# Kernel optimization log

Hardware: AMD Instinct MI355X
Metric: run time of the kernel (lower is better)

Reference implementation:

```python
import jax, jax.numpy as jnp
import numpy as np

B, C, N, K, COUT, W32 = 4, 64, 4096, 16, 64, 32
EPS = 1e-5  # BatchNorm eps


def conv1x1(x, w, b):
    # x: (B, Cin, K, N), w: (Cout, Cin), b: (Cout,)
    return jnp.einsum('oi,bikn->bokn', w, x) + b[None, :, None, None]


def batchnorm(x, gamma, beta):
    # training-mode BN over (B, K, N) per channel
    m = x.mean(axis=(0, 2, 3), keepdims=True)
    v = x.var(axis=(0, 2, 3), keepdims=True)
    return gamma[None, :, None, None] * (x - m) * jax.lax.rsqrt(v + EPS) + beta[None, :, None, None]


def setup_inputs() -> dict:
    key = jax.random.key(0)
    ks = jax.random.split(key, 14)
    s = 0.1
    return {
        'inputs': jax.random.normal(ks[0], (B, C, N), jnp.float32),
        'inputs_pos': jax.random.normal(ks[1], (B, 3, N), jnp.float32),
        'inverse_density': jax.random.uniform(ks[2], (B, 1, N), jnp.float32),
        # WeightNet: Conv2d(3, 32, 1) + BN(32)
        'wn_w': jax.random.normal(ks[3], (W32, 3), jnp.float32) * s,
        'wn_b': jnp.zeros((W32,), jnp.float32),
        'wn_g': jnp.ones((W32,), jnp.float32),
        'wn_be': jnp.zeros((W32,), jnp.float32),
        # DensityNet: Conv2d(1,16,1)+BN(16), Conv2d(16,1,1)
        'dn_w1': jax.random.normal(ks[4], (16, 1), jnp.float32) * s,
        'dn_b1': jnp.zeros((16,), jnp.float32),
        'dn_g1': jnp.ones((16,), jnp.float32),
        'dn_be1': jnp.zeros((16,), jnp.float32),
        'dn_w2': jax.random.normal(ks[5], (1, 16), jnp.float32) * s,
        'dn_b2': jnp.zeros((1,), jnp.float32),
        # Linear(C*32, COUT)
        'lin_w': jax.random.normal(ks[6], (COUT, C * W32), jnp.float32) * (1.0 / np.sqrt(C * W32)),
        'lin_b': jnp.zeros((COUT,), jnp.float32),
    }


def reference(inputs, inputs_pos, inverse_density,
              wn_w, wn_b, wn_g, wn_be,
              dn_w1, dn_b1, dn_g1, dn_be1, dn_w2, dn_b2,
              lin_w, lin_b):
    b, c, n = inputs.shape
    # pairwise squared distances (B, N, N); stride=1 so no FPS sampling
    sq = jnp.sum(inputs_pos ** 2, axis=1)  # (B, N)
    dist = sq[:, :, None] + sq[:, None, :] - 2.0 * jnp.einsum('bdi,bdj->bij', inputs_pos, inputs_pos)
    _, nn_idx = jax.lax.top_k(-dist, K)  # (B, N, K) nearest neighbors (incl. self)

    def gather(x, idx):  # x: (Cx, N), idx: (N, K) -> (Cx, K, N)
        return jnp.transpose(x[:, idx], (0, 2, 1))

    nn_pos = jax.vmap(gather)(inputs_pos, nn_idx)        # (B, 3, K, N)
    nn_inputs = jax.vmap(gather)(inputs, nn_idx)         # (B, C, K, N)
    lnn_pos = nn_pos - inputs_pos[:, :, None, :]         # translated neighbor positions
    nn_inv_d = jax.vmap(gather)(inverse_density, nn_idx)  # (B, 1, K, N)

    density_scale = nn_inv_d / nn_inv_d.max(axis=2, keepdims=True)
    h = jax.nn.relu(batchnorm(conv1x1(density_scale, dn_w1, dn_b1), dn_g1, dn_be1))
    density_scale = jax.nn.sigmoid(conv1x1(h, dn_w2, dn_b2))  # (B, 1, K, N)

    scaled = nn_inputs * density_scale                    # (B, C, K, N)
    weights = jax.nn.relu(batchnorm(conv1x1(lnn_pos, wn_w, wn_b), wn_g, wn_be))  # (B, 32, K, N)

    # per-point matmul: (B,N,C,K) @ (B,N,K,32) -> (B,N,C,32)
    feat = jnp.einsum('bckn,bwkn->bncw', scaled, weights).reshape(b, n, c * W32)
    out = feat @ lin_w.T + lin_b                          # (B, N, COUT)
    return jnp.transpose(out, (0, 2, 1))                  # (B, COUT, N)
```

## Files before the change

### kernel.cpp

```cpp
#include <hip/hip_runtime.h>
#include <math.h>

#define NB 4
#define NC 64
#define NPTS 4096
#define NROWS (NB*NPTS)

typedef __attribute__((ext_vector_type(4))) float f32x4;
typedef __bf16 bf16x8 __attribute__((ext_vector_type(8)));

__device__ __forceinline__ ushort f2bf(float f) {
  unsigned u = __float_as_uint(f);
  u = (u + 0x7FFFu + ((u >> 16) & 1u)) >> 16;
  return (ushort)u;
}
__device__ __forceinline__ unsigned pk2(float lo, float hi) {
  return (unsigned)f2bf(lo) | ((unsigned)f2bf(hi) << 16);
}

__device__ __forceinline__ void insert16(double dist, int j, double (&dd)[16], int (&ii)[16]) {
  double cd = dist; int ci = j;
#pragma unroll
  for (int s = 0; s < 16; ++s) {
    double od = dd[s]; int oi = ii[s];
    bool c = cd < od;
    dd[s] = c ? cd : od;
    ii[s] = c ? ci : oi;
    cd = c ? od : cd;
    ci = c ? oi : ci;
  }
}

__device__ __forceinline__ void bub24(unsigned key, unsigned (&top)[24]) {
#pragma unroll
  for (int q2 = 0; q2 < 24; ++q2) {
    unsigned lo = min(key, top[q2]);
    key = max(key, top[q2]);
    top[q2] = lo;
  }
}

__device__ __forceinline__ void bub16u(unsigned key, unsigned (&t)[16]) {
#pragma unroll
  for (int q2 = 0; q2 < 16; ++q2) {
    unsigned lo = min(key, t[q2]);
    key = max(key, t[q2]);
    t[q2] = lo;
  }
}

__device__ __forceinline__ double wave_reduce(double v) {
#pragma unroll
  for (int off = 32; off; off >>= 1) v += __shfl_down(v, off, 64);
  return v;
}

__global__ __launch_bounds__(256) void pack_pos4(const float* __restrict__ pos,
                                                 float4* __restrict__ pos4) {
  int g = blockIdx.x * 256 + threadIdx.x;
  int b = g >> 12, n = g & (NPTS - 1);
  const float* pb = pos + b * 3 * NPTS;
  pos4[g] = make_float4(pb[n], pb[NPTS + n], pb[2 * NPTS + n], 0.f);
}

__global__ __launch_bounds__(256) void knn_sub(const float4* __restrict__ pos4,
                                               uint4* __restrict__ partials) {
  __shared__ float4 cand[128];
  int t = threadIdx.x;
  int row0 = blockIdx.x * 256;
  int b = row0 >> 12;
  int y = blockIdx.y;
  int j0 = (y >> 1) * 1024 + (y & 1) * 128;
  const float4* pb = pos4 + b * NPTS;
  if (t < 128) cand[t] = pb[j0 + t];
  __syncthreads();
  float4 q = pb[(row0 + t) & (NPTS - 1)];
  unsigned dd[16];
#pragma unroll
  for (int s = 0; s < 16; ++s) dd[s] = 0xFFFFFFFFu;
#pragma unroll 4
  for (int jj = 0; jj < 128; ++jj) {
    float4 c = cand[jj];
    float dx = q.x - c.x, dy = q.y - c.y, dz = q.z - c.z;
    float d = fmaf(dx, dx, fmaf(dy, dy, dz * dz));
    unsigned key = (__float_as_uint(d) & 0xFFFFF000u) | (unsigned)(j0 + jj);
#pragma unroll
    for (int s = 0; s < 16; ++s) {
      unsigned lo = min(key, dd[s]);
      key = max(key, dd[s]);
      dd[s] = lo;
    }
  }
  uint4* po = partials + ((size_t)y * NROWS + row0 + t) * 4;
  po[0] = make_uint4(dd[0], dd[1], dd[2], dd[3]);
  po[1] = make_uint4(dd[4], dd[5], dd[6], dd[7]);
  po[2] = make_uint4(dd[8], dd[9], dd[10], dd[11]);
  po[3] = make_uint4(dd[12], dd[13], dd[14], dd[15]);
}

__global__ __launch_bounds__(64) void knn_thresh(const uint4* __restrict__ partials,
                                                 unsigned* __restrict__ T0g) {
  __shared__ unsigned sl[64 * 132];
  int tid = threadIdx.x;
  int row0 = blockIdx.x * 64;
  uint4* sl4 = (uint4*)sl;
  size_t base = (size_t)row0 * 4 + tid;
#define TW(IT, V) { int g2 = ((IT) & 3) * 64 + tid; \
                    sl4[(g2 >> 2) * 33 + ((IT) >> 2) * 4 + (g2 & 3)] = (V); }
#define TB(B) { int IT0 = (B) * 8; \
  uint4 w0 = partials[(size_t)((IT0+0)>>2)*(NROWS*4) + ((IT0+0)&3)*64 + base]; \
  uint4 w1 = partials[(size_t)((IT0+1)>>2)*(NROWS*4) + ((IT0+1)&3)*64 + base]; \
  uint4 w2 = partials[(size_t)((IT0+2)>>2)*(NROWS*4) + ((IT0+2)&3)*64 + base]; \
  uint4 w3 = partials[(size_t)((IT0+3)>>2)*(NROWS*4) + ((IT0+3)&3)*64 + base]; \
  uint4 w4 = partials[(size_t)((IT0+4)>>2)*(NROWS*4) + ((IT0+4)&3)*64 + base]; \
  uint4 w5 = partials[(size_t)((IT0+5)>>2)*(NROWS*4) + ((IT0+5)&3)*64 + base]; \
  uint4 w6 = partials[(size_t)((IT0+6)>>2)*(NROWS*4) + ((IT0+6)&3)*64 + base]; \
  uint4 w7 = partials[(size_t)((IT0+7)>>2)*(NROWS*4) + ((IT0+7)&3)*64 + base]; \
  TW(IT0+0,w0) TW(IT0+1,w1) TW(IT0+2,w2) TW(IT0+3,w3) \
  TW(IT0+4,w4) TW(IT0+5,w5) TW(IT0+6,w6) TW(IT0+7,w7) }
  TB(0) TB(1) TB(2) TB(3)
#undef TB
#undef TW
  __syncthreads();
  unsigned top[16];
#pragma unroll
  for (int s = 0; s < 16; ++s) top[s] = 0xFFFFFFFFu;
  const unsigned* my = sl + tid * 132;
  for (int y = 0; y < 8; ++y) {
#pragma unroll 4
    for (int s = 0; s < 16; ++s) {
      unsigned key = my[y * 16 + s];
      if (key >= top[15]) break;
#pragma unroll
      for (int q2 = 0; q2 < 16; ++q2) {
        unsigned lo = min(key, top[q2]);
        key = max(key, top[q2]);
        top[q2] = lo;
      }
    }
  }
  T0g[row0 + tid] = top[15] & 0xFFFFF000u;
}

__global__ __launch_bounds__(256) void knn_filter(const float4* __restrict__ pos4,
                                                  const unsigned* __restrict__ T0g,
                                                  uint4* __restrict__ surv) {
  __shared__ float4 cand[256];
  __shared__ unsigned lq[256 * 28];
  int t = threadIdx.x;
  int row0 = blockIdx.x * 256;
  int b = row0 >> 12;
  int y = blockIdx.y;
  int j0 = y * 256;
  const float4* pb = pos4 + b * NPTS;
  cand[t] = pb[j0 + t];
  __syncthreads();
  int r = row0 + t;
  float4 q = pb[r & (NPTS - 1)];
  unsigned T = T0g[r];
  unsigned cnt = 0;
  unsigned* myq = lq + t * 28;
#pragma unroll 4
  for (int jj = 0; jj < 256; ++jj) {
    float4 c = cand[jj];
    float dx = q.x - c.x, dy = q.y - c.y, dz = q.z - c.z;
    float d = fmaf(dx, dx, fmaf(dy, dy, dz * dz));
    unsigned m = __float_as_uint(d) & 0xFFFFF000u;
    if (m <= T) {
      if (cnt < 28u) myq[cnt] = m | (unsigned)(j0 + jj);
      ++cnt;
    }
  }
  cnt = cnt < 28u ? cnt : 28u;
  unsigned t16[16];
#pragma unroll
  for (int s = 0; s < 16; ++s) t16[s] = 0xFFFFFFFFu;
  const uint4* qsrc = (const uint4*)myq;
  uint4 q0 = qsrc[0], q1 = qsrc[1], q2 = qsrc[2], q3 = qsrc[3],
        q4 = qsrc[4], q5 = qsrc[5], q6 = qsrc[6];
#define SIN(K, I) { unsigned key = ((I) < cnt) ? (K) : 0xFFFFFFFFu; bub16u(key, t16); }
  SIN(q0.x,0u) SIN(q0.y,1u) SIN(q0.z,2u) SIN(q0.w,3u)
  SIN(q1.x,4u) SIN(q1.y,5u) SIN(q1.z,6u) SIN(q1.w,7u)
  SIN(q2.x,8u) SIN(q2.y,9u) SIN(q2.z,10u) SIN(q2.w,11u)
  SIN(q3.x,12u) SIN(q3.y,13u) SIN(q3.z,14u) SIN(q3.w,15u)
  SIN(q4.x,16u) SIN(q4.y,17u) SIN(q4.z,18u) SIN(q4.w,19u)
  SIN(q5.x,20u) SIN(q5.y,21u) SIN(q5.z,22u) SIN(q5.w,23u)
  SIN(q6.x,24u) SIN(q6.y,25u) SIN(q6.z,26u) SIN(q6.w,27u)
#undef SIN
  uint4* dst = surv + ((size_t)r * 16 + y) * 4;
  dst[0] = make_uint4(t16[0], t16[1], t16[2], t16[3]);
  dst[1] = make_uint4(t16[4], t16[5], t16[6], t16[7]);
  dst[2] = make_uint4(t16[8], t16[9], t16[10], t16[11]);
  dst[3] = make_uint4(t16[12], t16[13], t16[14], t16[15]);
}

__global__ __launch_bounds__(64) void knn_final(const float4* __restrict__ pos4,
                                                const float* __restrict__ invd,
                                                const uint4* __restrict__ surv,
                                                int* __restrict__ nn_idx,
                                                float* __restrict__ dsbuf,
                                                double* __restrict__ stp) {
  __shared__ unsigned sl[64 * 264];
  int tid = threadIdx.x;
  int row0 = blockIdx.x * 64;
  uint4* sl4 = (uint4*)sl;
  const uint4* sg = surv + (size_t)row0 * 64;
#define STW(G, V) { int rw = (G) >> 6, of = (G) & 63; sl4[rw * 66 + of] = (V); }
#define LDB(B) { int g0 = (B) * 512 + tid; \
  uint4 v0 = sg[g0], v1 = sg[g0 + 64], v2 = sg[g0 + 128], v3 = sg[g0 + 192], \
        v4 = sg[g0 + 256], v5 = sg[g0 + 320], v6 = sg[g0 + 384], v7 = sg[g0 + 448]; \
  STW(g0, v0) STW(g0 + 64, v1) STW(g0 + 128, v2) STW(g0 + 192, v3) \
  STW(g0 + 256, v4) STW(g0 + 320, v5) STW(g0 + 384, v6) STW(g0 + 448, v7) }
  LDB(0) LDB(1) LDB(2) LDB(3) LDB(4) LDB(5) LDB(6) LDB(7)
#undef LDB
#undef STW
  __syncthreads();

  int r = row0 + tid;
  int b = r >> 12, n = r & (NPTS - 1);

  unsigned top[24];
#pragma unroll
  for (int s = 0; s < 24; ++s) top[s] = 0xFFFFFFFFu;
  const unsigned* my = sl + tid * 264;
  for (int y = 0; y < 16; ++y) {
#pragma unroll 4
    for (int s = 0; s < 16; ++s) {
      unsigned key = my[y * 16 + s];
      if (key >= top[23]) break;
      bub24(key, top);
    }
  }

  const float4* pb = pos4 + b * NPTS;
  float4 qp = pb[n];
  double xi = qp.x, yi = qp.y, zi = qp.z;
  double dd[16]; int ii[16];
#pragma unroll
  for (int s = 0; s < 16; ++s) { dd[s] = 1e300; ii[s] = 0; }
#pragma unroll 4
  for (int s = 0; s < 24; ++s) {
    unsigned key = top[s];
    if (key != 0xFFFFFFFFu) {
      int j = (int)(key & 0xFFFu);
      float4 cj = pb[j];
      double dx = xi - (double)cj.x;
      double dy = yi - (double)cj.y;
      double dz = zi - (double)cj.z;
      double dist = dx * dx + dy * dy + dz * dz;
      if (dist < dd[15]) insert16(dist, j, dd, ii);
    }
  }

  const float* ivb = invd + b * NPTS;
  float xv[16];
  float vmax = -1e30f;
#pragma unroll
  for (int s = 0; s < 16; ++s) {
    int j = ii[s];
    nn_idx[(size_t)r * 16 + s] = j;
    float v = ivb[j];
    xv[s] = v;
    vmax = fmaxf(vmax, v);
  }
  double sx = 0, sxx = 0;
  double l1x = 0, l1y = 0, l1z = 0;
  double lxx = 0, lyy = 0, lzz = 0, lxy = 0, lxz = 0, lyz = 0;
#pragma unroll
  for (int s = 0; s < 16; ++s) {
    float x = xv[s] / vmax;
    dsbuf[(size_t)r * 16 + s] = x;
    sx += x; sxx += (double)x * (double)x;
    int j = ii[s];
    float4 cj = pb[j];
    double lx = (double)cj.x - xi;
    double ly = (double)cj.y - yi;
    double lz = (double)cj.z - zi;
    l1x += lx; l1y += ly; l1z += lz;
    lxx += lx * lx; lyy += ly * ly; lzz += lz * lz;
    lxy += lx * ly; lxz += lx * lz; lyz += ly * lz;
  }
  sx  = wave_reduce(sx);  sxx = wave_reduce(sxx);
  l1x = wave_reduce(l1x); l1y = wave_reduce(l1y); l1z = wave_reduce(l1z);
  lxx = wave_reduce(lxx); lyy = wave_reduce(lyy); lzz = wave_reduce(lzz);
  lxy = wave_reduce(lxy); lxz = wave_reduce(lxz); lyz = wave_reduce(lyz);
  if (tid == 0) {
    double* o = stp + (size_t)blockIdx.x * 16;
    o[0] = sx;  o[1] = sxx;
    o[2] = l1x; o[3] = l1y; o[4] = l1z;
    o[5] = lxx; o[6] = lyy; o[7] = lzz;
    o[8] = lxy; o[9] = lxz; o[10] = lyz;
  }
}

__global__ void finalize_params(const double* __restrict__ stp,
                                const float* __restrict__ wn_w,
                                const float* __restrict__ wn_g,
                                const float* __restrict__ wn_be,
                                const float* __restrict__ dn_w1,
                                const float* __restrict__ dn_g1,
                                const float* __restrict__ dn_be1,
                                float* __restrict__ prm) {
  __shared__ double red[11];
  const double M = (double)NROWS * 16.0;
  int t = threadIdx.x;
  if (t < 11) {
    double s = 0.0;
#pragma unroll 8
    for (int blk = 0; blk < 256; ++blk) s += stp[(size_t)blk * 16 + t];
    red[t] = s;
  }
  __syncthreads();
  if (t < 32) {
    double m0 = red[2] / M, m1 = red[3] / M, m2 = red[4] / M;
    double cxx = red[5] / M - m0 * m0, cyy = red[6] / M - m1 * m1, czz = red[7] / M - m2 * m2;
    double cxy = red[8] / M - m0 * m1, cxz = red[9] / M - m0 * m2, cyz = red[10] / M - m1 * m2;
    double w0 = wn_w[t * 3], w1 = wn_w[t * 3 + 1], w2 = wn_w[t * 3 + 2];
    double var = w0 * w0 * cxx + w1 * w1 * cyy + w2 * w2 * czz
               + 2.0 * (w0 * w1 * cxy + w0 * w2 * cxz + w1 * w2 * cyz);
    double alpha = (double)wn_g[t] / sqrt(var + 1e-5);
    double a0 = alpha * w0, a1 = alpha * w1, a2 = alpha * w2;
    prm[t * 3] = (float)a0; prm[t * 3 + 1] = (float)a1; prm[t * 3 + 2] = (float)a2;
    prm[96 + t] = (float)((double)wn_be[t] - (a0 * m0 + a1 * m1 + a2 * m2));
  } else if (t < 48) {
    int ch = t - 32;
    double mx = red[0] / M;
    double vx = red[1] / M - mx * mx;
    double w = dn_w1[ch];
    double alpha = (double)dn_g1[ch] * w / sqrt(w * w * vx + 1e-5);
    prm[128 + ch] = (float)alpha;
    prm[144 + ch] = (float)((double)dn_be1[ch] - alpha * mx);
  }
}

__global__ __launch_bounds__(256) void ds_kernel(float* __restrict__ dsbuf,
                                                 const float* __restrict__ prm,
                                                 const float* __restrict__ dn_w2,
                                                 const float* __restrict__ dn_b2) {
  int r = blockIdx.x * 256 + threadIdx.x;
  float A[16], Bp[16], W2[16];
#pragma unroll
  for (int ch = 0; ch < 16; ++ch) {
    A[ch] = prm[128 + ch];
    Bp[ch] = prm[144 + ch];
    W2[ch] = dn_w2[ch];
  }
  float b2 = dn_b2[0];
#pragma unroll
  for (int k = 0; k < 16; ++k) {
    float x = dsbuf[(size_t)r * 16 + k];
    float s = b2;
#pragma unroll
    for (int ch = 0; ch < 16; ++ch) s = fmaf(W2[ch], fmaxf(fmaf(A[ch], x, Bp[ch]), 0.f), s);
    dsbuf[(size_t)r * 16 + k] = 1.f / (1.f + expf(-s));
  }
}

__global__ __launch_bounds__(256) void transpose_in(const float* __restrict__ in,
                                                    ushort* __restrict__ inT) {
  __shared__ float tile[64][68];
  int t = threadIdx.x;
  int b = blockIdx.x >> 6;
  int n0 = (blockIdx.x & 63) << 6;
  {
    int c = t >> 2, q = t & 3;
    const float* src = in + ((size_t)(b * 64 + c)) * NPTS + n0 + q * 16;
    float4 v0 = ((const float4*)src)[0];
    float4 v1 = ((const float4*)src)[1];
    float4 v2 = ((const float4*)src)[2];
    float4 v3 = ((const float4*)src)[3];
    *(float4*)&tile[c][q * 16 + 0] = v0;
    *(float4*)&tile[c][q * 16 + 4] = v1;
    *(float4*)&tile[c][q * 16 + 8] = v2;
    *(float4*)&tile[c][q * 16 + 12] = v3;
  }
  __syncthreads();
  {
    int nl = t >> 2, cq = t & 3;
    unsigned pk[8];
#pragma unroll
    for (int i = 0; i < 8; ++i) {
      float lo = tile[cq * 16 + 2 * i][nl];
      float hi = tile[cq * 16 + 2 * i + 1][nl];
      pk[i] = pk2(lo, hi);
    }
    uint4* dst = (uint4*)(inT + ((size_t)(b * NPTS + n0 + nl)) * 64 + cq * 16);
    dst[0] = make_uint4(pk[0], pk[1], pk[2], pk[3]);
    dst[1] = make_uint4(pk[4], pk[5], pk[6], pk[7]);
  }
}

__global__ __launch_bounds__(256) void prep_LTf(const float* __restrict__ lin_w,
                                                ushort* __restrict__ LTf) {
  int g = blockIdx.x * 256 + threadIdx.x;
  int l = g & 63, ot = (g >> 6) & 3, s = g >> 8;
  int o = ot * 16 + (l & 15);
  const float* src = lin_w + (size_t)o * 2048 + s * 32 + (l >> 4) * 8;
  float4 u0 = ((const float4*)src)[0];
  float4 u1 = ((const float4*)src)[1];
  ((uint4*)LTf)[g] = make_uint4(pk2(u0.x, u0.y), pk2(u0.z, u0.w),
                                pk2(u1.x, u1.y), pk2(u1.z, u1.w));
}

#define XSTR 2320
#define WSTR 524

#define FMA_ROW(c) \
  a##c##_0 += W0 * (f32x4)x##c; a##c##_1 += W1 * (f32x4)x##c; \
  a##c##_2 += W2 * (f32x4)x##c; a##c##_3 += W3 * (f32x4)x##c; \
  a##c##_4 += W4 * (f32x4)x##c; a##c##_5 += W5 * (f32x4)x##c; \
  a##c##_6 += W6 * (f32x4)x##c; a##c##_7 += W7 * (f32x4)x##c;

#define WRITE_C(ci, csval) \
  { size_t base = ((size_t)(csval)) * 64 + pl; \
    aq[base +  0] = make_uint4(pk2(a##ci##_0.x, a##ci##_0.y), pk2(a##ci##_0.z, a##ci##_0.w), \
                               pk2(a##ci##_1.x, a##ci##_1.y), pk2(a##ci##_1.z, a##ci##_1.w)); \
    aq[base + 16] = make_uint4(pk2(a##ci##_2.x, a##ci##_2.y), pk2(a##ci##_2.z, a##ci##_2.w), \
                               pk2(a##ci##_3.x, a##ci##_3.y), pk2(a##ci##_3.z, a##ci##_3.w)); \
    aq[base + 32] = make_uint4(pk2(a##ci##_4.x, a##ci##_4.y), pk2(a##ci##_4.z, a##ci##_4.w), \
                               pk2(a##ci##_5.x, a##ci##_5.y), pk2(a##ci##_5.z, a##ci##_5.w)); \
    aq[base + 48] = make_uint4(pk2(a##ci##_6.x, a##ci##_6.y), pk2(a##ci##_6.z, a##ci##_6.w), \
                               pk2(a##ci##_7.x, a##ci##_7.y), pk2(a##ci##_7.z, a##ci##_7.w)); }

__global__ __launch_bounds__(256, 2) void fused(const ushort* __restrict__ inT,
                                                const float4* __restrict__ pos4,
                                                const int* __restrict__ nn_idx,
                                                const float* __restrict__ dsbuf,
                                                const float* __restrict__ prm_g,
                                                const ushort* __restrict__ LTf,
                                                const float* __restrict__ lin_b,
                                                float* __restrict__ out) {
  __shared__ __align__(16) char smem[16 * XSTR + 16 * WSTR * 4];
  __shared__ float prms[128];
  char* xraw = smem;
  float* wlds = (float*)(smem + 16 * XSTR);
  int t = threadIdx.x;
  int blk = blockIdx.x;
  int b = blk >> 8;
  int n0 = (blk & 255) << 4;
  if (t < 128) prms[t] = prm_g[t];
  __syncthreads();
  {
    int k = t >> 4, p = t & 15;
    int r = blk * 16 + p;
    int n = n0 + p;
    int j = nn_idx[(size_t)r * 16 + k];
    float4 pj = pos4[b * NPTS + j];
    float4 pn = pos4[b * NPTS + n];
    float lx = pj.x - pn.x, ly = pj.y - pn.y, lz = pj.z - pn.z;
    float ds = dsbuf[(size_t)r * 16 + k];
    const uint4* srcx = (const uint4*)(inT + ((size_t)(b * NPTS + j)) * 64);
    uint4* dstx = (uint4*)(xraw + p * XSTR + k * 144);
#pragma unroll
    for (int i = 0; i < 8; ++i) dstx[i] = srcx[i];
    float* wr = wlds + p * WSTR + k * 32;
#pragma unroll
    for (int w = 0; w < 32; ++w) {
      float v = fmaf(prms[w * 3], lx,
                fmaf(prms[w * 3 + 1], ly,
                fmaf(prms[w * 3 + 2], lz, prms[96 + w])));
      wr[w] = fmaxf(v, 0.f) * ds;
    }
  }
  __syncthreads();
  int pl = t & 15, cl = t >> 4;
  f32x4 a0_0=(f32x4)0.f, a0_1=(f32x4)0.f, a0_2=(f32x4)0.f, a0_3=(f32x4)0.f,
        a0_4=(f32x4)0.f, a0_5=(f32x4)0.f, a0_6=(f32x4)0.f, a0_7=(f32x4)0.f;
  f32x4 a1_0=(f32x4)0.f, a1_1=(f32x4)0.f, a1_2=(f32x4)0.f, a1_3=(f32x4)0.f,
        a1_4=(f32x4)0.f, a1_5=(f32x4)0.f, a1_6=(f32x4)0.f, a1_7=(f32x4)0.f;
  f32x4 a2_0=(f32x4)0.f, a2_1=(f32x4)0.f, a2_2=(f32x4)0.f, a2_3=(f32x4)0.f,
        a2_4=(f32x4)0.f, a2_5=(f32x4)0.f, a2_6=(f32x4)0.f, a2_7=(f32x4)0.f;
  f32x4 a3_0=(f32x4)0.f, a3_1=(f32x4)0.f, a3_2=(f32x4)0.f, a3_3=(f32x4)0.f,
        a3_4=(f32x4)0.f, a3_5=(f32x4)0.f, a3_6=(f32x4)0.f, a3_7=(f32x4)0.f;
  {
    const char* xrow = xraw + pl * XSTR;
    const float* wp = wlds + pl * WSTR;
#pragma unroll 4
    for (int kk = 0; kk < 16; ++kk) {
      unsigned xa = *(const unsigned*)(xrow + kk * 144 + cl * 4);
      unsigned xb = *(const unsigned*)(xrow + kk * 144 + 64 + cl * 4);
      float x0 = __uint_as_float(xa << 16);
      float x1 = __uint_as_float(xa & 0xFFFF0000u);
      float x2 = __uint_as_float(xb << 16);
      float x3 = __uint_as_float(xb & 0xFFFF0000u);
      const f32x4* wk = (const f32x4*)(wp + kk * 32);
      f32x4 W0 = wk[0], W1 = wk[1], W2 = wk[2], W3 = wk[3];
      f32x4 W4 = wk[4], W5 = wk[5], W6 = wk[6], W7 = wk[7];
      FMA_ROW(0)
      FMA_ROW(1)
      FMA_ROW(2)
      FMA_ROW(3)
    }
  }
  __syncthreads();
  uint4* aq = (uint4*)smem;
  WRITE_C(0, 2 * cl)
  WRITE_C(1, 2 * cl + 1)
  WRITE_C(2, 32 + 2 * cl)
  WRITE_C(3, 33 + 2 * cl)
  __syncthreads();
  {
    int wv = t >> 6, l = t & 63;
    const uint4* Lq = (const uint4*)LTf;
    f32x4 cacc = (f32x4)0.f;
#pragma unroll 4
    for (int s = 0; s < 64; ++s) {
      uint4 ua = aq[s * 64 + l];
      uint4 ub = Lq[(s * 4 + wv) * 64 + l];
      bf16x8 A = *reinterpret_cast<bf16x8*>(&ua);
      bf16x8 B = *reinterpret_cast<bf16x8*>(&ub);
      cacc = __builtin_amdgcn_mfma_f32_16x16x32_bf16(A, B, cacc, 0, 0, 0);
    }
    int o = wv * 16 + (l & 15);
    float bias = lin_b[o];
    cacc.x += bias; cacc.y += bias; cacc.z += bias; cacc.w += bias;
    *(f32x4*)(out + ((size_t)(b * 64 + o)) * NPTS + n0 + (l >> 4) * 4) = cacc;
  }
}

extern "C" void kernel_launch(void* const* d_in, const int* in_sizes, int n_in,
                              void* d_out, int out_size, void* d_ws, size_t ws_size,
                              hipStream_t stream) {
  (void)in_sizes; (void)n_in; (void)out_size; (void)ws_size;
  const float* inputs = (const float*)d_in[0];
  const float* pos    = (const float*)d_in[1];
  const float* invd   = (const float*)d_in[2];
  const float* wn_w   = (const float*)d_in[3];
  const float* wn_g   = (const float*)d_in[5];
  const float* wn_be  = (const float*)d_in[6];
  const float* dn_w1  = (const float*)d_in[7];
  const float* dn_g1  = (const float*)d_in[9];
  const float* dn_be1 = (const float*)d_in[10];
  const float* dn_w2  = (const float*)d_in[11];
  const float* dn_b2  = (const float*)d_in[12];
  const float* lin_w  = (const float*)d_in[13];
  const float* lin_b  = (const float*)d_in[14];
  float* outp = (float*)d_out;

  char* ws = (char*)d_ws;
  double*   stp      = (double*)(ws + 294912);
  float*    prm      = (float*)(ws + 1024);
  float4*   pos4     = (float4*)(ws + 4096);
  int*      nnidx    = (int*)(ws + (size_t)(1u << 19));
  float*    dsbuf    = (float*)(ws + (size_t)(3u << 19));
  ushort*   inT      = (ushort*)(ws + (size_t)(5u << 19));
  ushort*   LTf      = (ushort*)(ws + (size_t)(9u << 19));
  unsigned* T0g      = (unsigned*)(ws + (size_t)(19u << 18));
  uint4*    partials = (uint4*)(ws + (size_t)(11u << 19));
  uint4*    surv     = (uint4*)(ws + (size_t)(11u << 19));

  pack_pos4<<<64, 256, 0, stream>>>(pos, pos4);
  transpose_in<<<256, 256, 0, stream>>>(inputs, inT);
  prep_LTf<<<64, 256, 0, stream>>>(lin_w, LTf);
  knn_sub<<<dim3(64, 8), 256, 0, stream>>>(pos4, partials);
  knn_thresh<<<256, 64, 0, stream>>>(partials, T0g);
  knn_filter<<<dim3(64, 16), 256, 0, stream>>>(pos4, T0g, surv);
  knn_final<<<256, 64, 0, stream>>>(pos4, invd, surv, nnidx, dsbuf, stp);
  finalize_params<<<1, 64, 0, stream>>>(stp, wn_w, wn_g, wn_be, dn_w1, dn_g1, dn_be1, prm);
  ds_kernel<<<64, 256, 0, stream>>>(dsbuf, prm, dn_w2, dn_b2);
  fused<<<1024, 256, 0, stream>>>(inT, pos4, nnidx, dsbuf, prm, LTf, lin_b, outp);
}
```

Baseline: 167.3 us.

## Parallelize kNN final merge across 16 lanes per query row

knn_final now gives each query row 16 lanes instead of one thread. Each lane holds one sorted 16-key survivor list, and the 24 smallest keys come from a 16-way shuffle min-merge that replaces the serial bubble insert through shared memory. Per-neighbor output writes and statistics are spread across lanes, so finalize_params now reduces 4096 partial records in two stages with 256 threads. Every lane still runs the redundant 24-candidate double-precision rerank, and the merge costs 24 rounds of shuffles.

```diff
diff --git a/kernel.cpp b/kernel.cpp
--- a/kernel.cpp
+++ b/kernel.cpp
@@ -28,15 +28,6 @@
     ii[s] = c ? ci : oi;
     cd = c ? od : cd;
     ci = c ? oi : ci;
-  }
-}
-
-__device__ __forceinline__ void bub24(unsigned key, unsigned (&top)[24]) {
-#pragma unroll
-  for (int q2 = 0; q2 < 24; ++q2) {
-    unsigned lo = min(key, top[q2]);
-    key = max(key, top[q2]);
-    top[q2] = lo;
   }
 }
 
@@ -194,43 +185,39 @@
   dst[3] = make_uint4(t16[12], t16[13], t16[14], t16[15]);
 }
 
-__global__ __launch_bounds__(64) void knn_final(const float4* __restrict__ pos4,
-                                                const float* __restrict__ invd,
-                                                const uint4* __restrict__ surv,
-                                                int* __restrict__ nn_idx,
-                                                float* __restrict__ dsbuf,
-                                                double* __restrict__ stp) {
-  __shared__ unsigned sl[64 * 264];
-  int tid = threadIdx.x;
-  int row0 = blockIdx.x * 64;
-  uint4* sl4 = (uint4*)sl;
-  const uint4* sg = surv + (size_t)row0 * 64;
-#define STW(G, V) { int rw = (G) >> 6, of = (G) & 63; sl4[rw * 66 + of] = (V); }
-#define LDB(B) { int g0 = (B) * 512 + tid; \
-  uint4 v0 = sg[g0], v1 = sg[g0 + 64], v2 = sg[g0 + 128], v3 = sg[g0 + 192], \
-        v4 = sg[g0 + 256], v5 = sg[g0 + 320], v6 = sg[g0 + 384], v7 = sg[g0 + 448]; \
-  STW(g0, v0) STW(g0 + 64, v1) STW(g0 + 128, v2) STW(g0 + 192, v3) \
-  STW(g0 + 256, v4) STW(g0 + 320, v5) STW(g0 + 384, v6) STW(g0 + 448, v7) }
-  LDB(0) LDB(1) LDB(2) LDB(3) LDB(4) LDB(5) LDB(6) LDB(7)
-#undef LDB
-#undef STW
-  __syncthreads();
-
-  int r = row0 + tid;
+__global__ __launch_bounds__(256) void knn_final(const float4* __restrict__ pos4,
+                                                 const float* __restrict__ invd,
+                                                 const uint4* __restrict__ surv,
+                                                 int* __restrict__ nn_idx,
+                                                 float* __restrict__ dsbuf,
+                                                 double* __restrict__ stp) {
+  int t = threadIdx.x;
+  int ln = t & 15;
+  int r = blockIdx.x * 16 + (t >> 4);
   int b = r >> 12, n = r & (NPTS - 1);
 
-  unsigned top[24];
-#pragma unroll
-  for (int s = 0; s < 24; ++s) top[s] = 0xFFFFFFFFu;
-  const unsigned* my = sl + tid * 264;
-  for (int y = 0; y < 16; ++y) {
-#pragma unroll 4
-    for (int s = 0; s < 16; ++s) {
-      unsigned key = my[y * 16 + s];
-      if (key >= top[23]) break;
-      bub24(key, top);
-    }
-  }
+  const uint4* sp = surv + ((size_t)r * 16 + ln) * 4;
+  uint4 u0 = sp[0], u1 = sp[1], u2 = sp[2], u3 = sp[3];
+  unsigned h0=u0.x,h1=u0.y,h2=u0.z,h3=u0.w,h4=u1.x,h5=u1.y,h6=u1.z,h7=u1.w,
+           h8=u2.x,h9=u2.y,h10=u2.z,h11=u2.w,h12=u3.x,h13=u3.y,h14=u3.z,h15=u3.w;
+  unsigned t0,t1,t2,t3,t4,t5,t6,t7,t8,t9,t10,t11,t12,t13,t14,t15,
+           t16,t17,t18,t19,t20,t21,t22,t23;
+#define RND(TT) { unsigned m = h0; \
+  m = min(m, (unsigned)__shfl_xor((int)m, 1)); \
+  m = min(m, (unsigned)__shfl_xor((int)m, 2)); \
+  m = min(m, (unsigned)__shfl_xor((int)m, 4)); \
+  m = min(m, (unsigned)__shfl_xor((int)m, 8)); \
+  TT = m; bool pop = (h0 == m); \
+  h0 = pop ? h1 : h0;  h1 = pop ? h2 : h1;  h2 = pop ? h3 : h2; \
+  h3 = pop ? h4 : h3;  h4 = pop ? h5 : h4;  h5 = pop ? h6 : h5; \
+  h6 = pop ? h7 : h6;  h7 = pop ? h8 : h7;  h8 = pop ? h9 : h8; \
+  h9 = pop ? h10 : h9; h10 = pop ? h11 : h10; h11 = pop ? h12 : h11; \
+  h12 = pop ? h13 : h12; h13 = pop ? h14 : h13; h14 = pop ? h15 : h14; \
+  h15 = pop ? 0xFFFFFFFFu : h15; }
+  RND(t0) RND(t1) RND(t2) RND(t3) RND(t4) RND(t5) RND(t6) RND(t7)
+  RND(t8) RND(t9) RND(t10) RND(t11) RND(t12) RND(t13) RND(t14) RND(t15)
+  RND(t16) RND(t17) RND(t18) RND(t19) RND(t20) RND(t21) RND(t22) RND(t23)
+#undef RND
 
   const float4* pb = pos4 + b * NPTS;
   float4 qp = pb[n];
@@ -238,54 +225,42 @@
   double dd[16]; int ii[16];
 #pragma unroll
   for (int s = 0; s < 16; ++s) { dd[s] = 1e300; ii[s] = 0; }
-#pragma unroll 4
-  for (int s = 0; s < 24; ++s) {
-    unsigned key = top[s];
-    if (key != 0xFFFFFFFFu) {
-      int j = (int)(key & 0xFFFu);
-      float4 cj = pb[j];
-      double dx = xi - (double)cj.x;
-      double dy = yi - (double)cj.y;
-      double dz = zi - (double)cj.z;
-      double dist = dx * dx + dy * dy + dz * dz;
-      if (dist < dd[15]) insert16(dist, j, dd, ii);
-    }
-  }
-
+#define RRK(TT) if (TT != 0xFFFFFFFFu) { int j = (int)(TT & 0xFFFu); \
+  float4 cj = pb[j]; \
+  double dx = xi - (double)cj.x, dy = yi - (double)cj.y, dz = zi - (double)cj.z; \
+  double dist = dx * dx + dy * dy + dz * dz; \
+  if (dist < dd[15]) insert16(dist, j, dd, ii); }
+  RRK(t0) RRK(t1) RRK(t2) RRK(t3) RRK(t4) RRK(t5) RRK(t6) RRK(t7)
+  RRK(t8) RRK(t9) RRK(t10) RRK(t11) RRK(t12) RRK(t13) RRK(t14) RRK(t15)
+  RRK(t16) RRK(t17) RRK(t18) RRK(t19) RRK(t20) RRK(t21) RRK(t22) RRK(t23)
+#undef RRK
+
+  int jm = ii[0];
+#pragma unroll
+  for (int s = 1; s < 16; ++s) jm = (ln == s) ? ii[s] : jm;
+  nn_idx[(size_t)r * 16 + ln] = jm;
   const float* ivb = invd + b * NPTS;
-  float xv[16];
-  float vmax = -1e30f;
-#pragma unroll
-  for (int s = 0; s < 16; ++s) {
-    int j = ii[s];
-    nn_idx[(size_t)r * 16 + s] = j;
-    float v = ivb[j];
-    xv[s] = v;
-    vmax = fmaxf(vmax, v);
-  }
-  double sx = 0, sxx = 0;
-  double l1x = 0, l1y = 0, l1z = 0;
-  double lxx = 0, lyy = 0, lzz = 0, lxy = 0, lxz = 0, lyz = 0;
-#pragma unroll
-  for (int s = 0; s < 16; ++s) {
-    float x = xv[s] / vmax;
-    dsbuf[(size_t)r * 16 + s] = x;
-    sx += x; sxx += (double)x * (double)x;
-    int j = ii[s];
-    float4 cj = pb[j];
-    double lx = (double)cj.x - xi;
-    double ly = (double)cj.y - yi;
-    double lz = (double)cj.z - zi;
-    l1x += lx; l1y += ly; l1z += lz;
-    lxx += lx * lx; lyy += ly * ly; lzz += lz * lz;
-    lxy += lx * ly; lxz += lx * lz; lyz += ly * lz;
-  }
+  float v = ivb[jm];
+  float vmax = v;
+  vmax = fmaxf(vmax, __shfl_xor(vmax, 1));
+  vmax = fmaxf(vmax, __shfl_xor(vmax, 2));
+  vmax = fmaxf(vmax, __shfl_xor(vmax, 4));
+  vmax = fmaxf(vmax, __shfl_xor(vmax, 8));
+  float x = v / vmax;
+  dsbuf[(size_t)r * 16 + ln] = x;
+
+  double sx = x, sxx = (double)x * (double)x;
+  float4 pj = pb[jm];
+  double lx = (double)pj.x - xi, lyv = (double)pj.y - yi, lzv = (double)pj.z - zi;
+  double l1x = lx, l1y = lyv, l1z = lzv;
+  double lxx = lx * lx, lyy = lyv * lyv, lzz = lzv * lzv;
+  double lxy = lx * lyv, lxz = lx * lzv, lyz = lyv * lzv;
   sx  = wave_reduce(sx);  sxx = wave_reduce(sxx);
   l1x = wave_reduce(l1x); l1y = wave_reduce(l1y); l1z = wave_reduce(l1z);
   lxx = wave_reduce(lxx); lyy = wave_reduce(lyy); lzz = wave_reduce(lzz);
   lxy = wave_reduce(lxy); lxz = wave_reduce(lxz); lyz = wave_reduce(lyz);
-  if (tid == 0) {
-    double* o = stp + (size_t)blockIdx.x * 16;
+  if ((t & 63) == 0) {
+    double* o = stp + ((size_t)blockIdx.x * 4 + (t >> 6)) * 16;
     o[0] = sx;  o[1] = sxx;
     o[2] = l1x; o[3] = l1y; o[4] = l1z;
     o[5] = lxx; o[6] = lyy; o[7] = lzz;
@@ -293,7 +268,7 @@
   }
 }
 
-__global__ void finalize_params(const double* __restrict__ stp,
+__global__ __launch_bounds__(256) void finalize_params(const double* __restrict__ stp,
                                 const float* __restrict__ wn_w,
                                 const float* __restrict__ wn_g,
                                 const float* __restrict__ wn_be,
@@ -301,13 +276,22 @@
                                 const float* __restrict__ dn_g1,
                                 const float* __restrict__ dn_be1,
                                 float* __restrict__ prm) {
+  __shared__ double part[16][16];
   __shared__ double red[11];
   const double M = (double)NROWS * 16.0;
   int t = threadIdx.x;
+  {
+    int c = t & 15, ch = t >> 4;
+    double s = 0.0;
+#pragma unroll 8
+    for (int w = 0; w < 256; ++w) s += stp[(size_t)(ch * 256 + w) * 16 + c];
+    part[ch][c] = s;
+  }
+  __syncthreads();
   if (t < 11) {
     double s = 0.0;
-#pragma unroll 8
-    for (int blk = 0; blk < 256; ++blk) s += stp[(size_t)blk * 16 + t];
+#pragma unroll
+    for (int ch = 0; ch < 16; ++ch) s += part[ch][t];
     red[t] = s;
   }
   __syncthreads();
@@ -538,7 +522,6 @@
   float* outp = (float*)d_out;
 
   char* ws = (char*)d_ws;
-  double*   stp      = (double*)(ws + 294912);
   float*    prm      = (float*)(ws + 1024);
   float4*   pos4     = (float4*)(ws + 4096);
   int*      nnidx    = (int*)(ws + (size_t)(1u << 19));
@@ -546,6 +529,7 @@
   ushort*   inT      = (ushort*)(ws + (size_t)(5u << 19));
   ushort*   LTf      = (ushort*)(ws + (size_t)(9u << 19));
   unsigned* T0g      = (unsigned*)(ws + (size_t)(19u << 18));
+  double*   stp      = (double*)(ws + (size_t)(5u << 20));
   uint4*    partials = (uint4*)(ws + (size_t)(11u << 19));
   uint4*    surv     = (uint4*)(ws + (size_t)(11u << 19));
 
@@ -555,8 +539,8 @@
   knn_sub<<<dim3(64, 8), 256, 0, stream>>>(pos4, partials);
   knn_thresh<<<256, 64, 0, stream>>>(partials, T0g);
   knn_filter<<<dim3(64, 16), 256, 0, stream>>>(pos4, T0g, surv);
-  knn_final<<<256, 64, 0, stream>>>(pos4, invd, surv, nnidx, dsbuf, stp);
-  finalize_params<<<1, 64, 0, stream>>>(stp, wn_w, wn_g, wn_be, dn_w1, dn_g1, dn_be1, prm);
+  knn_final<<<1024, 256, 0, stream>>>(pos4, invd, surv, nnidx, dsbuf, stp);
+  finalize_params<<<1, 256, 0, stream>>>(stp, wn_w, wn_g, wn_be, dn_w1, dn_g1, dn_be1, prm);
   ds_kernel<<<64, 256, 0, stream>>>(dsbuf, prm, dn_w2, dn_b2);
   fused<<<1024, 256, 0, stream>>>(inT, pos4, nnidx, dsbuf, prm, LTf, lin_b, outp);
 }
```

Result: slower. 181.4 us (+8.4%).
